# Kernel tuning notes

Measured on AMD Instinct MI355X. Metric: run time of the kernel, lower is better.

## Reference

```python
import jax, jax.numpy as jnp
import numpy as np

B, S, D = 4, 4096, 2048
SCAN, STATE = 128, 16


def setup_inputs() -> dict:
    key = jax.random.key(0)
    ks = jax.random.split(key, 8)
    scale = 1.0 / np.sqrt(D)
    scale_s = 1.0 / np.sqrt(SCAN)
    x = jax.random.normal(ks[0], (B, S, D), dtype=jnp.float32)
    Wi = jax.random.normal(ks[1], (SCAN, D), dtype=jnp.float32) * scale
    Wo = jax.random.normal(ks[2], (D, SCAN), dtype=jnp.float32) * 0.02  # torch zero-inits; small random for nontrivial output
    A_log = jax.random.normal(ks[3], (SCAN, STATE), dtype=jnp.float32) * 0.1
    Wb = jax.random.normal(ks[4], (STATE, SCAN), dtype=jnp.float32) * scale_s
    Wc = jax.random.normal(ks[5], (STATE, SCAN), dtype=jnp.float32) * scale_s
    Wdt = jax.random.normal(ks[6], (SCAN, SCAN), dtype=jnp.float32) * scale_s
    b_dt = jnp.full((SCAN,), -3.0, dtype=jnp.float32)
    Wg = jax.random.normal(ks[7], (SCAN, D), dtype=jnp.float32) * scale
    return {"x": x, "Wi": Wi, "Wo": Wo, "A_log": A_log, "Wb": Wb,
            "Wc": Wc, "Wdt": Wdt, "b_dt": b_dt, "Wg": Wg}


def _selective_scan_ffn(x, Wi, Wo, A_log, Wb, Wc, Wdt, b_dt, Wg):
    z = jnp.einsum('bsd,nd->bsn', x, Wi)                      # [B,S,SCAN]
    gate = jax.nn.silu(jnp.einsum('bsd,nd->bsn', x, Wg))      # [B,S,SCAN]
    A = -jnp.exp(A_log)                                        # [SCAN,STATE]
    B_in = jnp.einsum('bsn,kn->bsk', z, Wb)                   # [B,S,STATE]
    C_in = jnp.einsum('bsn,kn->bsk', z, Wc)                   # [B,S,STATE]
    dt = jax.nn.softplus(jnp.einsum('bsn,mn->bsm', z, Wdt) + b_dt)  # [B,S,SCAN]
    A_bar = 1.0 + dt[..., None] * A                            # [B,S,SCAN,STATE]

    def step(state, inp):
        a_t, dt_t, z_t, b_t, c_t = inp
        # state: [B,SCAN,STATE]
        state = a_t * state + dt_t[..., None] * (z_t[..., None] * b_t[:, None, :])
        y = jnp.einsum('bnk,bk->bn', state, c_t)               # [B,SCAN]
        return state, y

    xs = (jnp.moveaxis(A_bar, 1, 0), jnp.moveaxis(dt, 1, 0),
          jnp.moveaxis(z, 1, 0), jnp.moveaxis(B_in, 1, 0), jnp.moveaxis(C_in, 1, 0))
    state0 = jnp.zeros((x.shape[0], Wi.shape[0], A_log.shape[1]), dtype=x.dtype)
    _, ys = jax.lax.scan(step, state0, xs)                     # [S,B,SCAN]
    y = jnp.moveaxis(ys, 0, 1) * gate                          # [B,S,SCAN]
    return jnp.einsum('bsn,dn->bsd', y, Wo)                    # [B,S,D]


def reference(x, Wi, Wo, A_log, Wb, Wc, Wdt, b_dt, Wg):
    return _selective_scan_ffn(x, Wi, Wo, A_log, Wb, Wc, Wdt, b_dt, Wg)
```

## Files before the change

### kernel.cpp

```cpp
#include <hip/hip_runtime.h>
#include <hip/hip_bf16.h>
#include <math.h>

using bf16 = __hip_bfloat16;
typedef __attribute__((ext_vector_type(8))) short bf16x8;
typedef __attribute__((ext_vector_type(8))) short short8;
typedef __attribute__((ext_vector_type(4))) float f32x4;

#define AS1 __attribute__((address_space(1)))
#define AS3 __attribute__((address_space(3)))

constexpr int BATCH = 4;
constexpr int SEQ   = 4096;
constexpr int DIM   = 2048;
constexpr int SCAN  = 128;
constexpr int STATE = 16;
constexpr int LCH   = 16;
constexpr int NCH   = SEQ / LCH;

__device__ __forceinline__ float bf2f(bf16 v) { return __bfloat162float(v); }
__device__ __forceinline__ bf16  f2bf(float v) { return __float2bfloat16(v); }

__device__ __forceinline__ int probe_dtype(const unsigned short* __restrict__ xp) {
  int cnt = 0;
  for (int i = 0; i < 512; ++i) {
    int e = (xp[i] >> 7) & 0xFF;
    cnt += (e >= 107 && e <= 147) ? 1 : 0;
  }
  return (cnt >= 410) ? 1 : 0;
}

__device__ __forceinline__ void conv_b(const void* src, bf16* dst, int n, int f,
                                       int gtid, int nt) {
  if (f) { const bf16* s = (const bf16*)src;  for (int i = gtid; i < n; i += nt) dst[i] = s[i]; }
  else   { const float* s = (const float*)src; for (int i = gtid; i < n; i += nt) dst[i] = f2bf(s[i]); }
}
__device__ __forceinline__ void conv_f(const void* src, float* dst, int n, int f,
                                       int gtid, int nt) {
  if (f) { const bf16* s = (const bf16*)src;  for (int i = gtid; i < n; i += nt) dst[i] = bf2f(s[i]); }
  else   { const float* s = (const float*)src; for (int i = gtid; i < n; i += nt) dst[i] = s[i]; }
}
__device__ __forceinline__ void conv_aneg(const void* src, float* dst, int n, int f,
                                          int gtid, int nt) {
  if (f) { const bf16* s = (const bf16*)src;  for (int i = gtid; i < n; i += nt) dst[i] = -expf(bf2f(s[i])); }
  else   { const float* s = (const float*)src; for (int i = gtid; i < n; i += nt) dst[i] = -expf(s[i]); }
}

__global__ __launch_bounds__(256) void kconv_w(
    const unsigned short* __restrict__ xprobe,
    const void* Wi, const void* Wg, const void* Wo, const void* Wdt,
    const void* Wb, const void* Wc, const void* bdt, const void* Alog,
    bf16* Wzg, bf16* Wob, bf16* Wdtb, bf16* Wbb, bf16* Wcb,
    float* bdtf, float* Anegf, int* __restrict__ flag) {
  int f = probe_dtype(xprobe);
  if (blockIdx.x == 0 && threadIdx.x == 0) *flag = f;
  int nt = gridDim.x * blockDim.x;
  int g  = blockIdx.x * blockDim.x + threadIdx.x;
  conv_b(Wi,  Wzg,               SCAN * DIM,  f, g, nt);
  conv_b(Wg,  Wzg + SCAN * DIM,  SCAN * DIM,  f, g, nt);
  conv_b(Wo,  Wob,  DIM * SCAN,  f, g, nt);
  conv_b(Wdt, Wdtb, SCAN * SCAN, f, g, nt);
  conv_b(Wb,  Wbb,  STATE * SCAN, f, g, nt);
  conv_b(Wc,  Wcb,  STATE * SCAN, f, g, nt);
  conv_f(bdt,  bdtf,  SCAN,          f, g, nt);
  conv_aneg(Alog, Anegf, SCAN * STATE, f, g, nt);
}

__device__ __forceinline__ int swzb(int row, int colbyte) {
  return row * 128 + (colbyte ^ ((row & 7) << 4));
}

struct ARegs { float4 v[4]; };

template <int F>
__device__ __forceinline__ ARegs loadA(const void* __restrict__ xin, size_t rowbase,
                                       int k0, int acx) {
  ARegs r;
  if (F) {
    const float4* s = (const float4*)((const bf16*)xin + rowbase + k0 + acx);
    r.v[0] = s[0]; r.v[1] = s[1];
  } else {
    const float4* s = (const float4*)((const float*)xin + rowbase + k0 + acx);
    r.v[0] = s[0]; r.v[1] = s[1]; r.v[2] = s[2]; r.v[3] = s[3];
  }
  return r;
}

template <int F>
__device__ __forceinline__ void writeA(char* abuf, int ar, int acx, const ARegs& rg) {
  int c0 = acx * 2;
  char* d0 = abuf + swzb(ar, c0);
  char* d1 = abuf + swzb(ar, c0 + 16);
  if (F) {
    *(float4*)d0 = rg.v[0];
    *(float4*)d1 = rg.v[1];
  } else {
    union { short8 s; bf16 b[8]; } u0, u1;
    const float* fv = (const float*)&rg.v[0];
#pragma unroll
    for (int i = 0; i < 8; ++i) u0.b[i] = f2bf(fv[i]);
#pragma unroll
    for (int i = 0; i < 8; ++i) u1.b[i] = f2bf(fv[8 + i]);
    *(short8*)d0 = u0.s;
    *(short8*)d1 = u1.s;
  }
}

__device__ __forceinline__ void stageB(const bf16* __restrict__ W, int k0,
                                       char* bbuf, int tid) {
  int w = tid >> 6;
#pragma unroll
  for (int i = 0; i < 8; ++i) {
    int off = i * 4096 + tid * 16;
    int r   = off >> 7;
    int cbl = off & 127;
    int cbs = cbl ^ ((r & 7) << 4);
    const bf16* src = W + (size_t)r * DIM + k0 + (cbs >> 1);
    char* lb = bbuf + i * 4096 + w * 1024;
    __builtin_amdgcn_global_load_lds((const AS1 void*)src, (AS3 void*)lb, 16, 0, 0);
  }
}

__device__ __forceinline__ void compute64x256(const char* abuf, const char* bbuf,
                                              int tid, f32x4 acc[4][4]) {
  int l = tid & 63, w = tid >> 6;
  int lr = l & 15, lk = (l >> 4) * 8;
#pragma unroll
  for (int kk = 0; kk < 64; kk += 32) {
    int cb = (kk + lk) * 2;
    bf16x8 a[4], b[4];
#pragma unroll
    for (int m = 0; m < 4; ++m)
      a[m] = *(const bf16x8*)(abuf + swzb(m * 16 + lr, cb));
#pragma unroll
    for (int n = 0; n < 4; ++n)
      b[n] = *(const bf16x8*)(bbuf + swzb(w * 64 + n * 16 + lr, cb));
#pragma unroll
    for (int m = 0; m < 4; ++m)
#pragma unroll
      for (int n = 0; n < 4; ++n)
        acc[m][n] = __builtin_amdgcn_mfma_f32_16x16x32_bf16(a[m], b[n], acc[m][n], 0, 0, 0);
  }
}

__device__ __forceinline__ void vm_wait12() { asm volatile("s_waitcnt vmcnt(12)" ::: "memory"); __builtin_amdgcn_sched_barrier(0); }
__device__ __forceinline__ void vm_wait10() { asm volatile("s_waitcnt vmcnt(10)" ::: "memory"); __builtin_amdgcn_sched_barrier(0); }
__device__ __forceinline__ void vm_wait0()  { asm volatile("s_waitcnt vmcnt(0)"  ::: "memory"); __builtin_amdgcn_sched_barrier(0); }
__device__ __forceinline__ void lgkm0_barrier() {
  asm volatile("s_waitcnt lgkmcnt(0)" ::: "memory");
  __builtin_amdgcn_sched_barrier(0);
  __builtin_amdgcn_s_barrier();
}

template <int F>
__device__ __forceinline__ void k1_main(const void* __restrict__ xin,
                                        const bf16* __restrict__ W,
                                        char* lds, size_t xrow, int ar, int acx,
                                        int tid, f32x4 acc[4][4]) {
  constexpr int NK = DIM / 64;
  constexpr int BUF = 40960;
  ARegs aH = loadA<F>(xin, xrow, 0, acx);
  stageB(W, 0, lds + 0 * BUF + 8192, tid);
  ARegs aN = loadA<F>(xin, xrow, 64, acx);
  stageB(W, 64, lds + 1 * BUF + 8192, tid);
  if (F) vm_wait10(); else vm_wait12();
  writeA<F>(lds + 0 * BUF, ar, acx, aH);
  aH = aN;
  lgkm0_barrier();

  for (int t = 0; t < NK; ++t) {
    char* curb = lds + (t % 3) * BUF;
    if (t + 2 < NK) {
      aN = loadA<F>(xin, xrow, (t + 2) * 64, acx);
      stageB(W, (t + 2) * 64, lds + ((t + 2) % 3) * BUF + 8192, tid);
    }
    compute64x256(curb, curb + 8192, tid, acc);
    if (t + 1 < NK) {
      if (t + 2 < NK) { if (F) vm_wait10(); else vm_wait12(); }
      else            { vm_wait0(); }
      writeA<F>(lds + ((t + 1) % 3) * BUF, ar, acx, aH);
      aH = aN;
      lgkm0_barrier();
    }
  }
}

__global__ __launch_bounds__(256) void k12_zg(const void* __restrict__ xin,
                                              const bf16* __restrict__ Wzg,
                                              const bf16* __restrict__ Wdtb,
                                              const bf16* __restrict__ Wbb,
                                              const bf16* __restrict__ Wcb,
                                              const float* __restrict__ bdtf,
                                              const float* __restrict__ Aneg,
                                              bf16* __restrict__ z,
                                              bf16* __restrict__ gate,
                                              float* __restrict__ dt,
                                              float* __restrict__ Bv,
                                              float* __restrict__ Cv,
                                              float* __restrict__ fin,
                                              float* __restrict__ apr,
                                              const int* __restrict__ flag) {
  __shared__ char lds[122880];
  int tid = threadIdx.x;
  int mb  = blockIdx.x;
  int m0  = mb * 64;
  int f   = *flag;
  int ar  = tid >> 2;
  int acx = (tid & 3) * 16;
  size_t xrow = ((size_t)m0 + ar) * DIM;

  f32x4 acc[4][4];
#pragma unroll
  for (int m = 0; m < 4; ++m)
#pragma unroll
    for (int n = 0; n < 4; ++n)
#pragma unroll
      for (int j = 0; j < 4; ++j) acc[m][n][j] = 0.f;

  if (f) k1_main<1>(xin, Wzg, lds, xrow, ar, acx, tid, acc);
  else   k1_main<0>(xin, Wzg, lds, xrow, ar, acx, tid, acc);

  __syncthreads();

  bf16  (*zl)[136]  = (bf16  (*)[136])(lds);
  bf16  (*wl)[136]  = (bf16  (*)[136])(lds + 17408);
  float (*dtl)[132] = (float (*)[132])(lds + 61440);
  float (*Blc)[16]  = (float (*)[16]) (lds + 95232);

  {
    int l = tid & 63, w = tid >> 6;
    int wcg = w * 64;
    int sel = wcg >> 7;
    int cbb = wcg & 127;
    int lr = l & 15, lj = (l >> 4) * 4;
    bf16* o = sel ? gate : z;
#pragma unroll
    for (int m = 0; m < 4; ++m)
#pragma unroll
      for (int n = 0; n < 4; ++n)
#pragma unroll
        for (int j = 0; j < 4; ++j) {
          int rowl = m * 16 + lj + j;
          int col  = cbb + n * 16 + lr;
          float v = acc[m][n][j];
          if (sel) v = v / (1.f + expf(-v));
          bf16 bv = f2bf(v);
          o[(size_t)(m0 + rowl) * SCAN + col] = bv;
          if (!sel) zl[rowl][col] = bv;
        }
  }
  for (int idx = tid; idx < 160 * 16; idx += 256) {
    int r = idx >> 4, c8 = (idx & 15) << 3;
    const bf16* src;
    if (r < 128)      src = Wdtb + r * 128;
    else if (r < 144) src = Wbb + (r - 128) * 128;
    else              src = Wcb + (r - 144) * 128;
    *(short8*)&wl[r][c8] = *(const short8*)(src + c8);
  }
  __syncthreads();

  {
    int l = tid & 63, w = tid >> 6;
    int lr = l & 15, lk = (l >> 4) * 8, lj = (l >> 4) * 4;
    f32x4 acc2[10];
#pragma unroll
    for (int n = 0; n < 10; ++n)
#pragma unroll
      for (int j = 0; j < 4; ++j) acc2[n][j] = 0.f;

#pragma unroll
    for (int kk = 0; kk < 128; kk += 32) {
      bf16x8 a = *(const bf16x8*)&zl[w * 16 + lr][kk + lk];
#pragma unroll
      for (int n = 0; n < 10; ++n) {
        bf16x8 bfr = *(const bf16x8*)&wl[n * 16 + lr][kk + lk];
        acc2[n] = __builtin_amdgcn_mfma_f32_16x16x32_bf16(a, bfr, acc2[n], 0, 0, 0);
      }
    }

#pragma unroll
    for (int n = 0; n < 10; ++n) {
      int o = n * 16 + lr;
#pragma unroll
      for (int j = 0; j < 4; ++j) {
        int row = w * 16 + lj + j;
        float v = acc2[n][j];
        if (o < 128) {
          v += bdtf[o];
          v = fmaxf(v, 0.f) + log1pf(expf(-fabsf(v)));
          dt[(size_t)(m0 + row) * SCAN + o] = v;
          dtl[row][o] = v;
        } else if (o < 144) {
          Bv[(size_t)(m0 + row) * STATE + (o - 128)] = v;
          Blc[row][o - 128] = v;
        } else {
          Cv[(size_t)(m0 + row) * STATE + (o - 144)] = v;
        }
      }
    }
  }
  __syncthreads();

  {
    int n  = tid & 127;
    int cp = tid >> 7;
    int b   = m0 >> 12;
    int ch0 = (m0 & 4095) >> 4;
    float A[STATE];
#pragma unroll
    for (int k = 0; k < STATE; ++k) A[k] = Aneg[n * STATE + k];

#pragma unroll
    for (int ci = 0; ci < 2; ++ci) {
      int cc = cp * 2 + ci;
      float st[STATE], ap[STATE];
#pragma unroll
      for (int k = 0; k < STATE; ++k) { st[k] = 0.f; ap[k] = 1.f; }
#pragma unroll
      for (int t = 0; t < LCH; ++t) {
        int row = cc * LCH + t;
        float d = dtl[row][n];
        float u = d * bf2f(zl[row][n]);
#pragma unroll
        for (int kg = 0; kg < 4; ++kg) {
          float4 B4 = *(const float4*)&Blc[row][kg * 4];
          float a;
          a = fmaf(d, A[kg*4+0], 1.f); st[kg*4+0] = fmaf(a, st[kg*4+0], u * B4.x); ap[kg*4+0] *= a;
          a = fmaf(d, A[kg*4+1], 1.f); st[kg*4+1] = fmaf(a, st[kg*4+1], u * B4.y); ap[kg*4+1] *= a;
          a = fmaf(d, A[kg*4+2], 1.f); st[kg*4+2] = fmaf(a, st[kg*4+2], u * B4.z); ap[kg*4+2] *= a;
          a = fmaf(d, A[kg*4+3], 1.f); st[kg*4+3] = fmaf(a, st[kg*4+3], u * B4.w); ap[kg*4+3] *= a;
        }
      }
      size_t base = ((size_t)b * NCH + (ch0 + cc)) * (STATE * SCAN) + n;
#pragma unroll
      for (int k = 0; k < STATE; ++k) {
        fin[base + k * SCAN] = st[k];
        apr[base + k * SCAN] = ap[k];
      }
    }
  }
}

__global__ __launch_bounds__(64) void k3b(const float* __restrict__ fin,
                                          float* __restrict__ apr) {
  int c  = blockIdx.x * 64 + threadIdx.x;
  int b  = c >> 11;
  int kn = c & 2047;
  size_t base = (size_t)b * NCH * 2048 + kn;
  float s = 0.f;
  for (int g = 0; g < NCH; g += 16) {
    float fv[16], av[16];
#pragma unroll
    for (int i = 0; i < 16; ++i) {
      size_t o = base + (size_t)(g + i) * 2048;
      fv[i] = fin[o];
      av[i] = apr[o];
    }
#pragma unroll
    for (int i = 0; i < 16; ++i) {
      size_t o = base + (size_t)(g + i) * 2048;
      apr[o] = s;
      s = fmaf(av[i], s, fv[i]);
    }
  }
}

__global__ __launch_bounds__(128) void k3c(
    const float* __restrict__ dt, const bf16* z,
    const float* __restrict__ Bv, const float* __restrict__ Cv,
    const float* __restrict__ Aneg, const float* __restrict__ inc,
    const bf16* __restrict__ gate, bf16* yg) {
  __shared__ float Bl[LCH][STATE];
  __shared__ float Cl[LCH][STATE];
  int n  = threadIdx.x;
  int ch = blockIdx.x, b = blockIdx.y;
  int t0 = ch * LCH;
  if (n < LCH * STATE / 4)
    ((float4*)&Bl[0][0])[n] = ((const float4*)(Bv + ((size_t)b * SEQ + t0) * STATE))[n];
  else if (n < LCH * STATE / 2)
    ((float4*)&Cl[0][0])[n - LCH * STATE / 4] =
        ((const float4*)(Cv + ((size_t)b * SEQ + t0) * STATE))[n - LCH * STATE / 4];

  size_t base = ((size_t)b * NCH + ch) * (STATE * SCAN) + n;
  float A[STATE], st[STATE];
#pragma unroll
  for (int k = 0; k < STATE; ++k) {
    A[k]  = Aneg[n * STATE + k];
    st[k] = inc[base + k * SCAN];
  }
  __syncthreads();

  const float* dtp = dt   + ((size_t)b * SEQ + t0) * SCAN + n;
  const bf16*  zp  = z    + ((size_t)b * SEQ + t0) * SCAN + n;
  const bf16*  gp  = gate + ((size_t)b * SEQ + t0) * SCAN + n;
  bf16*        yp  = yg   + ((size_t)b * SEQ + t0) * SCAN + n;
#pragma unroll 4
  for (int t = 0; t < LCH; ++t) {
    float d = dtp[t * SCAN];
    float u = d * bf2f(zp[t * SCAN]);
    float g = bf2f(gp[t * SCAN]);
    float y0 = 0.f, y1 = 0.f, y2 = 0.f, y3 = 0.f;
#pragma unroll
    for (int kg = 0; kg < 4; ++kg) {
      float4 B4 = *(const float4*)&Bl[t][kg * 4];
      float4 C4 = *(const float4*)&Cl[t][kg * 4];
      float a, p = 0.f;
      a = fmaf(d, A[kg*4+0], 1.f); st[kg*4+0] = fmaf(a, st[kg*4+0], u * B4.x); p = fmaf(st[kg*4+0], C4.x, p);
      a = fmaf(d, A[kg*4+1], 1.f); st[kg*4+1] = fmaf(a, st[kg*4+1], u * B4.y); p = fmaf(st[kg*4+1], C4.y, p);
      a = fmaf(d, A[kg*4+2], 1.f); st[kg*4+2] = fmaf(a, st[kg*4+2], u * B4.z); p = fmaf(st[kg*4+2], C4.z, p);
      a = fmaf(d, A[kg*4+3], 1.f); st[kg*4+3] = fmaf(a, st[kg*4+3], u * B4.w); p = fmaf(st[kg*4+3], C4.w, p);
      if (kg == 0) y0 = p; else if (kg == 1) y1 = p; else if (kg == 2) y2 = p; else y3 = p;
    }
    float y = (y0 + y1) + (y2 + y3);
    yp[t * SCAN] = f2bf(y * g);
  }
}

__device__ __forceinline__ int swz256(int row, int colbyte) {
  return row * 256 + (colbyte ^ ((row & 7) << 4));
}

__global__ __launch_bounds__(256) void k4_out(const bf16* __restrict__ yg,
                                              const bf16* __restrict__ Wo,
                                              void* __restrict__ outv,
                                              const int* __restrict__ flag) {
  __shared__ char lds[49152];
  int tid = threadIdx.x;
  int mb = blockIdx.x, nb = blockIdx.y;
  int w = tid >> 6;

#pragma unroll
  for (int i = 0; i < 8; ++i) {
    int off = i * 4096 + tid * 16;
    int r   = off >> 8;
    int cbl = off & 255;
    int cbs = cbl ^ ((r & 7) << 4);
    const bf16* src = yg + (size_t)(mb * 128 + r) * SCAN + (cbs >> 1);
    __builtin_amdgcn_global_load_lds((const AS1 void*)src,
                                     (AS3 void*)(lds + i * 4096 + w * 1024), 16, 0, 0);
  }
#pragma unroll
  for (int i = 0; i < 4; ++i) {
    int off = i * 4096 + tid * 16;
    int r   = off >> 8;
    int cbl = off & 255;
    int cbs = cbl ^ ((r & 7) << 4);
    const bf16* src = Wo + (size_t)(nb * 64 + r) * SCAN + (cbs >> 1);
    __builtin_amdgcn_global_load_lds((const AS1 void*)src,
                                     (AS3 void*)(lds + 32768 + i * 4096 + w * 1024), 16, 0, 0);
  }
  __syncthreads();

  int l = tid & 63;
  int lr = l & 15, lk = (l >> 4) * 8;
  f32x4 acc[2][4];
#pragma unroll
  for (int m = 0; m < 2; ++m)
#pragma unroll
    for (int n = 0; n < 4; ++n)
#pragma unroll
      for (int j = 0; j < 4; ++j) acc[m][n][j] = 0.f;

#pragma unroll
  for (int kk = 0; kk < 128; kk += 32) {
    int cb = (kk + lk) * 2;
    bf16x8 a[2], b[4];
#pragma unroll
    for (int m = 0; m < 2; ++m)
      a[m] = *(const bf16x8*)(lds + swz256(w * 32 + m * 16 + lr, cb));
#pragma unroll
    for (int n = 0; n < 4; ++n)
      b[n] = *(const bf16x8*)(lds + 32768 + swz256(n * 16 + lr, cb));
#pragma unroll
    for (int m = 0; m < 2; ++m)
#pragma unroll
      for (int n = 0; n < 4; ++n)
        acc[m][n] = __builtin_amdgcn_mfma_f32_16x16x32_bf16(a[m], b[n], acc[m][n], 0, 0, 0);
  }

  int f = *flag;
  int lj = (l >> 4) * 4;
#pragma unroll
  for (int m = 0; m < 2; ++m)
#pragma unroll
    for (int n = 0; n < 4; ++n)
#pragma unroll
      for (int j = 0; j < 4; ++j) {
        int row = mb * 128 + w * 32 + m * 16 + lj + j;
        int col = nb * 64 + n * 16 + lr;
        size_t off = (size_t)row * DIM + col;
        float v = acc[m][n][j];
        if (f) ((bf16*)outv)[off] = f2bf(v);
        else   ((float*)outv)[off] = v;
      }
}

extern "C" void kernel_launch(void* const* d_in, const int* in_sizes, int n_in,
                              void* d_out, int out_size, void* d_ws, size_t ws_size,
                              hipStream_t stream) {
  const void* x     = d_in[0];
  const void* Wi    = d_in[1];
  const void* Wo    = d_in[2];
  const void* A_log = d_in[3];
  const void* Wb    = d_in[4];
  const void* Wc    = d_in[5];
  const void* Wdt   = d_in[6];
  const void* b_dt  = d_in[7];
  const void* Wg    = d_in[8];

  const size_t M = (size_t)BATCH * SEQ;
  char* p = (char*)d_ws;
  int*   flag = (int*)p;    p += 256;
  bf16*  Wzg  = (bf16*)p;   p += (size_t)2 * SCAN * DIM * 2;
  bf16*  Wob  = (bf16*)p;   p += (size_t)DIM * SCAN * 2;
  bf16*  Wdtb = (bf16*)p;   p += (size_t)SCAN * SCAN * 2;
  bf16*  Wbb  = (bf16*)p;   p += (size_t)STATE * SCAN * 2;
  bf16*  Wcb  = (bf16*)p;   p += (size_t)STATE * SCAN * 2;
  float* bdtf = (float*)p;  p += SCAN * 4;
  float* Anegf= (float*)p;  p += (size_t)SCAN * STATE * 4;
  bf16*  z    = (bf16*)p;   p += M * SCAN * 2;
  bf16*  gate = (bf16*)p;   p += M * SCAN * 2;
  bf16*  yg   = z;
  float* dt   = (float*)p;  p += M * SCAN * 4;
  float* Bv   = (float*)p;  p += M * STATE * 4;
  float* Cv   = (float*)p;  p += M * STATE * 4;
  float* fin  = (float*)p;  p += (size_t)BATCH * NCH * SCAN * STATE * 4;
  float* apr  = (float*)p;  p += (size_t)BATCH * NCH * SCAN * STATE * 4;

  kconv_w <<<256, 256, 0, stream>>>((const unsigned short*)x,
                                    Wi, Wg, Wo, Wdt, Wb, Wc, b_dt, A_log,
                                    Wzg, Wob, Wdtb, Wbb, Wcb, bdtf, Anegf, flag);
  k12_zg  <<<dim3(256), 256, 0, stream>>>(x, Wzg, Wdtb, Wbb, Wcb, bdtf, Anegf,
                                          z, gate, dt, Bv, Cv, fin, apr, flag);
  k3b     <<<dim3(128), 64, 0, stream>>>(fin, apr);
  k3c     <<<dim3(NCH, BATCH), 128, 0, stream>>>(dt, z, Bv, Cv, Anegf, apr, gate, yg);
  k4_out  <<<dim3(128, 32), 256, 0, stream>>>(yg, Wob, d_out, flag);
}
```

Before: 160.8 us.

## Split z/gate GEMM across block pairs and shrink LDS with bf16 scan staging

The fused input-projection kernel now launches twice as many blocks. Each pair of blocks handles one 64-row tile, with one block computing z (then running dt/B/C and the chunk scan) and the other computing the gate only and exiting early. Per-block LDS drops from about 120KB to about 77KB: the B tile is halved and the dt and B values kept in LDS for the scan are stored as bf16 instead of fp32. The goal is more parallelism and occupancy across CUs. The cost is that x is read twice, gate blocks sit idle during the scan phase, and bf16 rounding of dt and B feeding the scan adds numerical error.

```diff
diff --git a/kernel.cpp b/kernel.cpp
--- a/kernel.cpp
+++ b/kernel.cpp
@@ -20,6 +20,9 @@
 
 __device__ __forceinline__ float bf2f(bf16 v) { return __bfloat162float(v); }
 __device__ __forceinline__ bf16  f2bf(float v) { return __float2bfloat16(v); }
+__device__ __forceinline__ float bfbits(unsigned short u) {
+  return __uint_as_float((unsigned)u << 16);
+}
 
 __device__ __forceinline__ int probe_dtype(const unsigned short* __restrict__ xp) {
   int cnt = 0;
@@ -110,7 +113,7 @@
                                        char* bbuf, int tid) {
   int w = tid >> 6;
 #pragma unroll
-  for (int i = 0; i < 8; ++i) {
+  for (int i = 0; i < 4; ++i) {
     int off = i * 4096 + tid * 16;
     int r   = off >> 7;
     int cbl = off & 127;
@@ -121,31 +124,32 @@
   }
 }
 
-__device__ __forceinline__ void compute64x256(const char* abuf, const char* bbuf,
-                                              int tid, f32x4 acc[4][4]) {
+__device__ __forceinline__ void compute64x128(const char* abuf, const char* bbuf,
+                                              int tid, f32x4 acc[4][2]) {
   int l = tid & 63, w = tid >> 6;
+  int wc = w * 32;
   int lr = l & 15, lk = (l >> 4) * 8;
 #pragma unroll
   for (int kk = 0; kk < 64; kk += 32) {
     int cb = (kk + lk) * 2;
-    bf16x8 a[4], b[4];
+    bf16x8 a[4], b[2];
 #pragma unroll
     for (int m = 0; m < 4; ++m)
       a[m] = *(const bf16x8*)(abuf + swzb(m * 16 + lr, cb));
 #pragma unroll
-    for (int n = 0; n < 4; ++n)
-      b[n] = *(const bf16x8*)(bbuf + swzb(w * 64 + n * 16 + lr, cb));
+    for (int n = 0; n < 2; ++n)
+      b[n] = *(const bf16x8*)(bbuf + swzb(wc + n * 16 + lr, cb));
 #pragma unroll
     for (int m = 0; m < 4; ++m)
 #pragma unroll
-      for (int n = 0; n < 4; ++n)
+      for (int n = 0; n < 2; ++n)
         acc[m][n] = __builtin_amdgcn_mfma_f32_16x16x32_bf16(a[m], b[n], acc[m][n], 0, 0, 0);
   }
 }
 
-__device__ __forceinline__ void vm_wait12() { asm volatile("s_waitcnt vmcnt(12)" ::: "memory"); __builtin_amdgcn_sched_barrier(0); }
-__device__ __forceinline__ void vm_wait10() { asm volatile("s_waitcnt vmcnt(10)" ::: "memory"); __builtin_amdgcn_sched_barrier(0); }
-__device__ __forceinline__ void vm_wait0()  { asm volatile("s_waitcnt vmcnt(0)"  ::: "memory"); __builtin_amdgcn_sched_barrier(0); }
+__device__ __forceinline__ void vm_wait8() { asm volatile("s_waitcnt vmcnt(8)" ::: "memory"); __builtin_amdgcn_sched_barrier(0); }
+__device__ __forceinline__ void vm_wait6() { asm volatile("s_waitcnt vmcnt(6)" ::: "memory"); __builtin_amdgcn_sched_barrier(0); }
+__device__ __forceinline__ void vm_wait0() { asm volatile("s_waitcnt vmcnt(0)" ::: "memory"); __builtin_amdgcn_sched_barrier(0); }
 __device__ __forceinline__ void lgkm0_barrier() {
   asm volatile("s_waitcnt lgkmcnt(0)" ::: "memory");
   __builtin_amdgcn_sched_barrier(0);
@@ -156,14 +160,14 @@
 __device__ __forceinline__ void k1_main(const void* __restrict__ xin,
                                         const bf16* __restrict__ W,
                                         char* lds, size_t xrow, int ar, int acx,
-                                        int tid, f32x4 acc[4][4]) {
+                                        int tid, f32x4 acc[4][2]) {
   constexpr int NK = DIM / 64;
-  constexpr int BUF = 40960;
+  constexpr int BUF = 24576;
   ARegs aH = loadA<F>(xin, xrow, 0, acx);
   stageB(W, 0, lds + 0 * BUF + 8192, tid);
   ARegs aN = loadA<F>(xin, xrow, 64, acx);
   stageB(W, 64, lds + 1 * BUF + 8192, tid);
-  if (F) vm_wait10(); else vm_wait12();
+  if (F) vm_wait6(); else vm_wait8();
   writeA<F>(lds + 0 * BUF, ar, acx, aH);
   aH = aN;
   lgkm0_barrier();
@@ -174,9 +178,9 @@
       aN = loadA<F>(xin, xrow, (t + 2) * 64, acx);
       stageB(W, (t + 2) * 64, lds + ((t + 2) % 3) * BUF + 8192, tid);
     }
-    compute64x256(curb, curb + 8192, tid, acc);
+    compute64x128(curb, curb + 8192, tid, acc);
     if (t + 1 < NK) {
-      if (t + 2 < NK) { if (F) vm_wait10(); else vm_wait12(); }
+      if (t + 2 < NK) { if (F) vm_wait6(); else vm_wait8(); }
       else            { vm_wait0(); }
       writeA<F>(lds + ((t + 1) % 3) * BUF, ar, acx, aH);
       aH = aN;
@@ -200,48 +204,44 @@
                                               float* __restrict__ fin,
                                               float* __restrict__ apr,
                                               const int* __restrict__ flag) {
-  __shared__ char lds[122880];
+  __shared__ char lds[78336];
   int tid = threadIdx.x;
-  int mb  = blockIdx.x;
+  int bx  = blockIdx.x;
+  int mb  = bx >> 1;
+  int sel = bx & 1;
   int m0  = mb * 64;
   int f   = *flag;
   int ar  = tid >> 2;
   int acx = (tid & 3) * 16;
   size_t xrow = ((size_t)m0 + ar) * DIM;
-
-  f32x4 acc[4][4];
+  const bf16* W = Wzg + (size_t)sel * SCAN * DIM;
+
+  f32x4 acc[4][2];
 #pragma unroll
   for (int m = 0; m < 4; ++m)
 #pragma unroll
-    for (int n = 0; n < 4; ++n)
+    for (int n = 0; n < 2; ++n)
 #pragma unroll
       for (int j = 0; j < 4; ++j) acc[m][n][j] = 0.f;
 
-  if (f) k1_main<1>(xin, Wzg, lds, xrow, ar, acx, tid, acc);
-  else   k1_main<0>(xin, Wzg, lds, xrow, ar, acx, tid, acc);
-
-  __syncthreads();
-
-  bf16  (*zl)[136]  = (bf16  (*)[136])(lds);
-  bf16  (*wl)[136]  = (bf16  (*)[136])(lds + 17408);
-  float (*dtl)[132] = (float (*)[132])(lds + 61440);
-  float (*Blc)[16]  = (float (*)[16]) (lds + 95232);
-
+  if (f) k1_main<1>(xin, W, lds, xrow, ar, acx, tid, acc);
+  else   k1_main<0>(xin, W, lds, xrow, ar, acx, tid, acc);
+
+  bf16 (*zl)[128] = (bf16 (*)[128])(lds);
+  if (sel == 0) __syncthreads();
   {
     int l = tid & 63, w = tid >> 6;
-    int wcg = w * 64;
-    int sel = wcg >> 7;
-    int cbb = wcg & 127;
+    int wc = w * 32;
     int lr = l & 15, lj = (l >> 4) * 4;
     bf16* o = sel ? gate : z;
 #pragma unroll
     for (int m = 0; m < 4; ++m)
 #pragma unroll
-      for (int n = 0; n < 4; ++n)
+      for (int n = 0; n < 2; ++n)
 #pragma unroll
         for (int j = 0; j < 4; ++j) {
           int rowl = m * 16 + lj + j;
-          int col  = cbb + n * 16 + lr;
+          int col  = wc + n * 16 + lr;
           float v = acc[m][n][j];
           if (sel) v = v / (1.f + expf(-v));
           bf16 bv = f2bf(v);
@@ -249,6 +249,12 @@
           if (!sel) zl[rowl][col] = bv;
         }
   }
+  if (sel) return;
+
+  bf16 (*wl)[136]   = (bf16 (*)[136])(lds + 16384);
+  bf16 (*dtlb)[128] = (bf16 (*)[128])(lds + 59904);
+  bf16 (*Blcb)[16]  = (bf16 (*)[16]) (lds + 76288);
+
   for (int idx = tid; idx < 160 * 16; idx += 256) {
     int r = idx >> 4, c8 = (idx & 15) << 3;
     const bf16* src;
@@ -289,10 +295,10 @@
           v += bdtf[o];
           v = fmaxf(v, 0.f) + log1pf(expf(-fabsf(v)));
           dt[(size_t)(m0 + row) * SCAN + o] = v;
-          dtl[row][o] = v;
+          dtlb[row][o] = f2bf(v);
         } else if (o < 144) {
           Bv[(size_t)(m0 + row) * STATE + (o - 128)] = v;
-          Blc[row][o - 128] = v;
+          Blcb[row][o - 128] = f2bf(v);
         } else {
           Cv[(size_t)(m0 + row) * STATE + (o - 144)] = v;
         }
@@ -319,16 +325,20 @@
 #pragma unroll
       for (int t = 0; t < LCH; ++t) {
         int row = cc * LCH + t;
-        float d = dtl[row][n];
+        float d = bf2f(dtlb[row][n]);
         float u = d * bf2f(zl[row][n]);
 #pragma unroll
         for (int kg = 0; kg < 4; ++kg) {
-          float4 B4 = *(const float4*)&Blc[row][kg * 4];
+          unsigned long long bb = *(const unsigned long long*)&Blcb[row][kg * 4];
+          float b0 = bfbits((unsigned short)bb);
+          float b1 = bfbits((unsigned short)(bb >> 16));
+          float b2 = bfbits((unsigned short)(bb >> 32));
+          float b3 = bfbits((unsigned short)(bb >> 48));
           float a;
-          a = fmaf(d, A[kg*4+0], 1.f); st[kg*4+0] = fmaf(a, st[kg*4+0], u * B4.x); ap[kg*4+0] *= a;
-          a = fmaf(d, A[kg*4+1], 1.f); st[kg*4+1] = fmaf(a, st[kg*4+1], u * B4.y); ap[kg*4+1] *= a;
-          a = fmaf(d, A[kg*4+2], 1.f); st[kg*4+2] = fmaf(a, st[kg*4+2], u * B4.z); ap[kg*4+2] *= a;
-          a = fmaf(d, A[kg*4+3], 1.f); st[kg*4+3] = fmaf(a, st[kg*4+3], u * B4.w); ap[kg*4+3] *= a;
+          a = fmaf(d, A[kg*4+0], 1.f); st[kg*4+0] = fmaf(a, st[kg*4+0], u * b0); ap[kg*4+0] *= a;
+          a = fmaf(d, A[kg*4+1], 1.f); st[kg*4+1] = fmaf(a, st[kg*4+1], u * b1); ap[kg*4+1] *= a;
+          a = fmaf(d, A[kg*4+2], 1.f); st[kg*4+2] = fmaf(a, st[kg*4+2], u * b2); ap[kg*4+2] *= a;
+          a = fmaf(d, A[kg*4+3], 1.f); st[kg*4+3] = fmaf(a, st[kg*4+3], u * b3); ap[kg*4+3] *= a;
         }
       }
       size_t base = ((size_t)b * NCH + (ch0 + cc)) * (STATE * SCAN) + n;
@@ -530,7 +540,7 @@
   kconv_w <<<256, 256, 0, stream>>>((const unsigned short*)x,
                                     Wi, Wg, Wo, Wdt, Wb, Wc, b_dt, A_log,
                                     Wzg, Wob, Wdtb, Wbb, Wcb, bdtf, Anegf, flag);
-  k12_zg  <<<dim3(256), 256, 0, stream>>>(x, Wzg, Wdtb, Wbb, Wcb, bdtf, Anegf,
+  k12_zg  <<<dim3(512), 256, 0, stream>>>(x, Wzg, Wdtb, Wbb, Wcb, bdtf, Anegf,
                                           z, gate, dt, Bv, Cv, fin, apr, flag);
   k3b     <<<dim3(128), 64, 0, stream>>>(fin, apr);
   k3c     <<<dim3(NCH, BATCH), 128, 0, stream>>>(dt, z, Bv, Cv, Anegf, apr, gate, yg);
```

Measured after the change: 185.3 us. 1.15x slower.
